# Kernel optimization log

Hardware: AMD Instinct MI355X
Metric: run time of the kernel (lower is better)

Reference implementation:

```python
import jax, jax.numpy as jnp
import numpy as np

DT = 0.1
DEATH_THRESHOLD = 0.05


def setup_inputs() -> dict:
    key = jax.random.key(0)
    ks = jax.random.split(key, 12)
    B, S, DE, DM, DC, DEPTH = 1, 4096, 256, 64, 64, 4
    DIN = DE + DC
    w_scale = 0.02  # keeps pre-softmax scores in a sane range
    return {
        "e": jax.random.normal(ks[0], (B, S, DE), jnp.float32),
        "E": jax.random.uniform(ks[1], (B, S, 1), jnp.float32),
        "P": jax.random.uniform(ks[2], (B, S, 1), jnp.float32),
        "G": jax.random.normal(ks[3], (B, S, 1), jnp.float32),
        "m": jax.random.uniform(ks[4], (B, S, DM), jnp.float32),
        "c": jax.random.normal(ks[5], (B, S, DC), jnp.float32),
        "l": jax.random.uniform(ks[6], (B, S, 1), jnp.float32),
        "wq": jax.random.normal(ks[7], (DEPTH, DIN, DE), jnp.float32) * w_scale,
        "bq": jnp.zeros((DEPTH, DE), jnp.float32),
        "wk": jax.random.normal(ks[8], (DEPTH, DIN, DE), jnp.float32) * w_scale,
        "bk": jnp.zeros((DEPTH, DE), jnp.float32),
        "wv": jax.random.normal(ks[9], (DEPTH, DIN, DE), jnp.float32) * w_scale,
        "bv": jnp.zeros((DEPTH, DE), jnp.float32),
        "alpha": jnp.full((DEPTH,), 1.0, jnp.float32),
        "beta": jnp.full((DEPTH,), 0.5, jnp.float32),
        "gamma": jnp.full((DEPTH,), 0.2, jnp.float32),
        "basal": jnp.full((DEPTH,), 0.05, jnp.float32),
    }


def reference(e, E, P, G, m, c, l, wq, bq, wk, bk, wv, bv, alpha, beta, gamma, basal):
    depth = wq.shape[0]
    scale = 1.0 / np.sqrt(wq.shape[-1]).astype(np.float32)
    for i in range(depth):
        # --- OuterTrans: multiplicatively-masked self-attention ---
        x = jnp.concatenate([e, c], axis=-1)                 # [B,S,DE+DC]
        q = x @ wq[i] + bq[i]
        k = x @ wk[i] + bk[i]
        v = x @ wv[i] + bv[i]
        scores = jnp.einsum("bsd,btd->bst", q, k) * scale    # [B,S,S]
        membrane = jnp.einsum("bsd,btd->bst", m, m)          # [B,S,S]
        lifespan = jnp.einsum("bsd,btd->bst", l, l)          # [B,S,S]
        attn = jax.nn.softmax(scores * membrane * lifespan, axis=-1)
        h_tilde = jnp.einsum("bst,btd->bsd", attn, v)        # [B,S,DE]
        e = e + h_tilde
        # --- ThermodynamicODE (elementwise per-token update) ---
        S_in = jnp.sum(h_tilde * h_tilde, axis=-1, keepdims=True)  # ||h||^2 [B,S,1]
        PE = P * E
        P_new = jax.nn.relu(P + (alpha[i] * S_in - beta[i] * PE) * DT)
        E_new = jax.nn.relu(E + (basal[i] - gamma[i] * PE) * DT)
        m_target = jax.nn.sigmoid(E_new - P_new)             # [B,S,1] broadcast to m
        G = G + (0.1 * E_new - 0.5 * P_new) * DT
        l_decay = 0.01 + 0.5 * jax.nn.relu(P_new - 2.0)
        m = 0.9 * m + 0.1 * m_target
        l = jnp.clip(l - l_decay * DT, 0.0, 1.0)
        E, P = E_new, P_new
    # Dynamic pruning: jit-compatible variant -> zero-mask dead cells instead of
    # data-dependent slicing; also return alive_mask and num_died.
    alive = l > DEATH_THRESHOLD                              # [B,S,1] bool
    af = alive.astype(e.dtype)
    num_died = e.shape[1] - jnp.sum(alive.astype(jnp.int32))
    return (e * af, E * af, P * af, G * af, m * af, c * af, l * af,
            alive[0, :, 0], num_died)
```

## Files before the change

kernel.cpp:

```cpp
#include <hip/hip_runtime.h>
#include <hip/hip_bf16.h>
#include <math.h>

#define SS 4096
#define DE 256
#define DM 64
#define DC 64
#define DIN 320
#define DEPTH 4
#define DT_C 0.1f
#define NSPLIT 12
#define BK 32
#define EXP_SHIFT 8.0f

typedef float f32x4_t __attribute__((ext_vector_type(4)));
typedef __bf16 bf16x8_t __attribute__((ext_vector_type(8)));

#define MFMA_BF16(A, B, C) __builtin_amdgcn_mfma_f32_16x16x32_bf16((A), (B), (C), 0, 0, 0)

#define OFF_E     (SS*DE)
#define OFF_P     (OFF_E + SS)
#define OFF_G     (OFF_P + SS)
#define OFF_M     (OFF_G + SS)
#define OFF_C     (OFF_M + SS*DM)
#define OFF_L     (OFF_C + SS*DM)
#define OFF_ALIVE (OFF_L + SS)
#define OFF_DIED  (OFF_ALIVE + SS)

#define WS_EWS   0
#define WS_MWS   (WS_EWS  + SS*DE)
#define WS_EE    (WS_MWS  + SS*DM)
#define WS_PP    (WS_EE   + SS)
#define WS_GG    (WS_PP   + SS)
#define WS_LL    (WS_GG   + SS)
#define WS_PL    (WS_LL   + SS)
#define WS_POB   (WS_PL   + NSPLIT*SS)
#define WS_XB    (WS_POB  + NSPLIT*SS*DE/2)
#define WS_QB    (WS_XB   + SS*DIN/2)
#define WS_KB    (WS_QB   + SS*DE/2)
#define WS_VTB   (WS_KB   + SS*DE/2)
#define WS_MB    (WS_VTB  + SS*DE/2)
#define WS_WT    (WS_MB   + SS*DM/2)
#define WS_SEM   (WS_WT   + 3*DEPTH*DE*DIN/2)

#define KT_STR 264
#define VT_STR 40

__global__ __launch_bounds__(256) void transpose_w_kernel(
    const float* __restrict__ wq, const float* __restrict__ wk, const float* __restrict__ wv,
    __hip_bfloat16* __restrict__ wt)
{
    const int zd = blockIdx.z;
    const int z = zd >> 2;
    const float* src = (z == 0 ? wq : (z == 1 ? wk : wv)) + (size_t)(zd & 3) * DIN * DE;
    __shared__ float t[32][33];
    const int k0 = blockIdx.x * 32;
    const int n0 = blockIdx.y * 32;
    const int tr = threadIdx.x >> 5;
    const int tc = threadIdx.x & 31;
    #pragma unroll
    for (int p = 0; p < 4; ++p)
        t[p*8 + tr][tc] = src[(size_t)(k0 + p*8 + tr) * DE + n0 + tc];
    __syncthreads();
    #pragma unroll
    for (int p = 0; p < 4; ++p) {
        int n = n0 + p*8 + tr;
        int k = k0 + tc;
        wt[((size_t)zd * DE + n) * DIN + k] = __float2bfloat16(t[tc][p*8 + tr]);
    }
}

__global__ __launch_bounds__(256) void init_kernel(
    const float* __restrict__ e_in, const float* __restrict__ c_in,
    const float* __restrict__ E_in, const float* __restrict__ P_in,
    const float* __restrict__ G_in, const float* __restrict__ l_in,
    const float* __restrict__ m_in,
    float* __restrict__ e_ws, __hip_bfloat16* __restrict__ xb,
    float* __restrict__ E_ws, float* __restrict__ P_ws, float* __restrict__ G_ws,
    float* __restrict__ l_ws, float* __restrict__ m_ws, __hip_bfloat16* __restrict__ mb,
    int* __restrict__ counters)
{
    const int row = blockIdx.x;
    const int tid = threadIdx.x;
    const float v = e_in[(size_t)row * DE + tid];
    e_ws[(size_t)row * DE + tid] = v;
    xb[(size_t)row * DIN + tid] = __float2bfloat16(v);
    if (tid < DC) {
        xb[(size_t)row * DIN + DE + tid] = __float2bfloat16(c_in[(size_t)row * DC + tid]);
        const float mv = m_in[(size_t)row * DM + tid];
        m_ws[(size_t)row * DM + tid] = mv;
        mb[(size_t)row * DM + tid] = __float2bfloat16(mv);
    }
    if (tid == 0) {
        E_ws[row] = E_in[row];
        P_ws[row] = P_in[row];
        G_ws[row] = G_in[row];
        l_ws[row] = l_in[row];
    }
    if (row == 0 && tid < 2) counters[tid] = 0;
}

__global__ __launch_bounds__(256, 2) void projc_kernel(
    const __hip_bfloat16* __restrict__ part_ob, const float* __restrict__ part_l,
    float* __restrict__ e_ws, __hip_bfloat16* __restrict__ xb,
    float* __restrict__ E_ws, float* __restrict__ P_ws, float* __restrict__ G_ws,
    float* __restrict__ m_ws, __hip_bfloat16* __restrict__ mb, float* __restrict__ l_ws,
    const float* __restrict__ alpha, const float* __restrict__ beta,
    const float* __restrict__ gamma_, const float* __restrict__ basal,
    const __hip_bfloat16* __restrict__ wt,
    const float* __restrict__ bq, const float* __restrict__ bk, const float* __restrict__ bv,
    __hip_bfloat16* __restrict__ qb, __hip_bfloat16* __restrict__ kb, __hip_bfloat16* __restrict__ vtb,
    int layer)
{
    const int id = blockIdx.x;
    const int xcd = id & 7, inner = id >> 3;
    const int qblk = (xcd << 3) | (inner >> 2);
    const int rb = qblk * 4 + (inner & 3);
    const int tid = threadIdx.x;

    if (layer > 0) {
        const int wc = tid >> 6, lane = tid & 63;
        const int lp = layer - 1;
        const float a = alpha[lp], bb = beta[lp], gm = gamma_[lp], bas = basal[lp];
        #pragma unroll
        for (int rr = 0; rr < 4; ++rr) {
            const int row = rb * 16 + wc * 4 + rr;
            const int qb2 = row >> 6, wa = (row >> 4) & 3, quada = (row >> 2) & 3, ra = row & 3;
            float L = 0.f;
            #pragma unroll
            for (int s = 0; s < NSPLIT; ++s) L += part_l[s * SS + row];
            const float invL = 1.0f / L;
            const int ct = lane >> 2;
            const int base_off = (ct * 64 + quada * 16 + (lane & 3) * 4) * 4;
            float o[4] = {0.f, 0.f, 0.f, 0.f};
            #pragma unroll
            for (int s = 0; s < NSPLIT; ++s) {
                const size_t region = ((size_t)((s * (SS / 64) + qb2) * 4 + wa)) * 4096;
                const ushort* pp = (const ushort*)(part_ob + region) + base_off;
                ushort vals[16];
                *(uint4*)&vals[0] = *(const uint4*)pp;
                *(uint4*)&vals[8] = *(const uint4*)(pp + 8);
                #pragma unroll
                for (int j = 0; j < 4; ++j)
                    o[j] += __uint_as_float(((unsigned)vals[j * 4 + ra]) << 16);
            }
            const float h0 = o[0] * invL, h1 = o[1] * invL, h2 = o[2] * invL, h3 = o[3] * invL;
            float4 ev = *(float4*)&e_ws[(size_t)row * DE + lane * 4];
            ev.x += h0; ev.y += h1; ev.z += h2; ev.w += h3;
            *(float4*)&e_ws[(size_t)row * DE + lane * 4] = ev;
            __hip_bfloat16 x4[4] = {__float2bfloat16(ev.x), __float2bfloat16(ev.y),
                                    __float2bfloat16(ev.z), __float2bfloat16(ev.w)};
            *(uint2*)&xb[(size_t)row * DIN + lane * 4] = *(uint2*)x4;

            float ssq = h0*h0 + h1*h1 + h2*h2 + h3*h3;
            #pragma unroll
            for (int mask = 1; mask < 64; mask <<= 1) ssq += __shfl_xor(ssq, mask);

            const float E = E_ws[row], P = P_ws[row];
            const float PE = P * E;
            const float Pn = fmaxf(0.f, P + (a * ssq - bb * PE) * DT_C);
            const float En = fmaxf(0.f, E + (bas - gm * PE) * DT_C);
            const float mtg = 1.f / (1.f + __expf(-(En - Pn)));
            const size_t mi = (size_t)row * DM + lane;
            const float mv = 0.9f * m_ws[mi] + 0.1f * mtg;
            m_ws[mi] = mv;
            mb[mi] = __float2bfloat16(mv);
            if (lane == 0) {
                E_ws[row] = En;
                P_ws[row] = Pn;
                G_ws[row] = G_ws[row] + (0.1f * En - 0.5f * Pn) * DT_C;
                const float ldec = 0.01f + 0.5f * fmaxf(0.f, Pn - 2.0f);
                const float lv = l_ws[row] - ldec * DT_C;
                l_ws[row] = fminf(1.f, fmaxf(0.f, lv));
            }
        }
        __syncthreads();
    }

    const int w = tid >> 6, lane = tid & 63;
    const int m = lane & 15, quad = lane >> 4;
    const int row0 = rb * 16;

    bf16x8_t xa[10];
    #pragma unroll
    for (int kk = 0; kk < 10; ++kk)
        xa[kk] = *(const bf16x8_t*)&xb[(size_t)(row0 + m) * DIN + kk * 32 + quad * 8];

    f32x4_t acc[12];
    #pragma unroll
    for (int nt = 0; nt < 12; ++nt) acc[nt] = (f32x4_t){0.f, 0.f, 0.f, 0.f};

    #pragma unroll
    for (int kk = 0; kk < 10; ++kk) {
        #pragma unroll
        for (int nt = 0; nt < 12; ++nt) {
            const int gcol = w * 192 + nt * 16 + m;
            const int z = gcol >> 8, col = gcol & 255;
            bf16x8_t bfrag = *(const bf16x8_t*)&wt[((size_t)(z * DEPTH + layer) * DE + col) * DIN + kk * 32 + quad * 8];
            acc[nt] = MFMA_BF16(xa[kk], bfrag, acc[nt]);
        }
    }
    #pragma unroll
    for (int nt = 0; nt < 12; ++nt) {
        const int gcol = w * 192 + nt * 16 + m;
        const int z = gcol >> 8, col = gcol & 255;
        const float* bias = (z == 0 ? bq : (z == 1 ? bk : bv)) + (size_t)layer * DE;
        const float b = bias[col];
        #pragma unroll
        for (int r = 0; r < 4; ++r) {
            const int row = row0 + quad * 4 + r;
            const __hip_bfloat16 h = __float2bfloat16(acc[nt][r] + b);
            if (z == 0)      qb[(size_t)row * DE + col] = h;
            else if (z == 1) kb[(size_t)row * DE + col] = h;
            else             vtb[(size_t)col * SS + row] = h;
        }
    }
}

__global__ __launch_bounds__(256, 3) void attn_mfma_kernel(
    const __hip_bfloat16* __restrict__ qb, const __hip_bfloat16* __restrict__ kb,
    const __hip_bfloat16* __restrict__ vtb, const __hip_bfloat16* __restrict__ mb,
    const float* __restrict__ l_ws,
    __hip_bfloat16* __restrict__ part_ob, float* __restrict__ part_l)
{
    __shared__ __align__(16) __hip_bfloat16 kt[32 * KT_STR];
    __shared__ __align__(16) __hip_bfloat16 vt[256 * VT_STR];

    const int id = blockIdx.x;
    const int split = id >> 6;
    const int rid = id & 63;
    const int qblk = (rid & 7) * 8 + (rid >> 3);

    const int tid = threadIdx.x;
    const int w = tid >> 6, lane = tid & 63;
    const int n = lane & 15, quad = lane >> 4;
    const int row0 = qblk * 64 + w * 16;

    bf16x8_t qa[8];
    #pragma unroll
    for (int kk = 0; kk < 8; ++kk)
        qa[kk] = *(const bf16x8_t*)&qb[(size_t)(row0 + n) * DE + kk * 32 + quad * 8];
    bf16x8_t ma[2];
    #pragma unroll
    for (int kk = 0; kk < 2; ++kk)
        ma[kk] = *(const bf16x8_t*)&mb[(size_t)(row0 + n) * DM + kk * 32 + quad * 8];
    const float lqs = l_ws[row0 + n] * 0.0625f;

    f32x4_t oacc[16];
    #pragma unroll
    for (int ct = 0; ct < 16; ++ct) oacc[ct] = (f32x4_t){0.f, 0.f, 0.f, 0.f};
    float plsum = 0.f;
    const f32x4_t zf4 = (f32x4_t){0.f, 0.f, 0.f, 0.f};

    const int k_row = tid >> 5, k_g = tid & 31;
    const int v_col = tid >> 2, v_seg = tid & 3;
    const int v_base = (v_seg & 1) * 16 + (v_seg >> 1) * 4;

    const int it_begin = (split * 128) / NSPLIT;
    const int it_end   = ((split + 1) * 128) / NSPLIT;

    for (int it = it_begin; it < it_end; ++it) {
        const int t0 = it * BK;
        __syncthreads();
        #pragma unroll
        for (int p = 0; p < 4; ++p) {
            const int row = k_row + p * 8;
            *(float4*)&kt[row * KT_STR + k_g * 8] = *(const float4*)&kb[(size_t)(t0 + row) * DE + k_g * 8];
        }
        #pragma unroll
        for (int p = 0; p < 4; ++p) {
            const int col = v_col + p * 64;
            const float4 f = *(const float4*)&vtb[(size_t)col * SS + t0 + v_seg * 8];
            *(float2*)&vt[col * VT_STR + v_base]     = make_float2(f.x, f.y);
            *(float2*)&vt[col * VT_STR + v_base + 8] = make_float2(f.z, f.w);
        }
        __syncthreads();

        const bf16x8_t mf00 = *(const bf16x8_t*)&mb[(size_t)(t0 + n) * DM + quad * 8];
        const bf16x8_t mf01 = *(const bf16x8_t*)&mb[(size_t)(t0 + n) * DM + 32 + quad * 8];
        const bf16x8_t mf10 = *(const bf16x8_t*)&mb[(size_t)(t0 + n + 16) * DM + quad * 8];
        const bf16x8_t mf11 = *(const bf16x8_t*)&mb[(size_t)(t0 + n + 16) * DM + 32 + quad * 8];
        const float4 lk0 = *(const float4*)&l_ws[t0 + quad * 4];
        const float4 lk1 = *(const float4*)&l_ws[t0 + 16 + quad * 4];

        f32x4_t s0a = zf4, s0b = zf4, s1a = zf4, s1b = zf4;
        #pragma unroll
        for (int kk = 0; kk < 4; ++kk) {
            bf16x8_t k0 = *(const bf16x8_t*)&kt[n * KT_STR + kk * 32 + quad * 8];
            bf16x8_t k1 = *(const bf16x8_t*)&kt[(n + 16) * KT_STR + kk * 32 + quad * 8];
            s0a = MFMA_BF16(k0, qa[kk], s0a);
            s1a = MFMA_BF16(k1, qa[kk], s1a);
        }
        #pragma unroll
        for (int kk = 4; kk < 8; ++kk) {
            bf16x8_t k0 = *(const bf16x8_t*)&kt[n * KT_STR + kk * 32 + quad * 8];
            bf16x8_t k1 = *(const bf16x8_t*)&kt[(n + 16) * KT_STR + kk * 32 + quad * 8];
            s0b = MFMA_BF16(k0, qa[kk], s0b);
            s1b = MFMA_BF16(k1, qa[kk], s1b);
        }
        const f32x4_t st0 = s0a + s0b;
        const f32x4_t st1 = s1a + s1b;

        f32x4_t mm0 = MFMA_BF16(mf00, ma[0], zf4);
        mm0 = MFMA_BF16(mf01, ma[1], mm0);
        f32x4_t mm1 = MFMA_BF16(mf10, ma[0], zf4);
        mm1 = MFMA_BF16(mf11, ma[1], mm1);

        bf16x8_t pa;
        #pragma unroll
        for (int r = 0; r < 4; ++r) {
            const float x0 = st0[r] * lqs * lk0[r] * mm0[r];
            const float x1 = st1[r] * lqs * lk1[r] * mm1[r];
            const float p0 = __expf(x0 - EXP_SHIFT);
            const float p1 = __expf(x1 - EXP_SHIFT);
            plsum += p0 + p1;
            pa[r]     = (__bf16)p0;
            pa[4 + r] = (__bf16)p1;
        }

        #pragma unroll
        for (int ct = 0; ct < 16; ++ct) {
            bf16x8_t vb = *(const bf16x8_t*)&vt[(ct * 16 + n) * VT_STR + quad * 8];
            oacc[ct] = MFMA_BF16(pa, vb, oacc[ct]);
        }
    }

    plsum += __shfl_xor(plsum, 16);
    plsum += __shfl_xor(plsum, 32);
    if (lane < 16)
        part_l[split * SS + row0 + lane] = plsum;

    __hip_bfloat16* dst = part_ob + ((size_t)((split * (SS / 64) + qblk) * 4 + w)) * 4096;
    #pragma unroll
    for (int ct = 0; ct < 16; ++ct) {
        __hip_bfloat16 h4[4];
        #pragma unroll
        for (int r = 0; r < 4; ++r) h4[r] = __float2bfloat16(oacc[ct][r]);
        *(uint2*)&dst[(ct * 64 + lane) * 4] = *(uint2*)h4;
    }
}

__global__ __launch_bounds__(256) void finalizec_kernel(
    const __hip_bfloat16* __restrict__ part_ob, const float* __restrict__ part_l,
    const float* __restrict__ e_ws,
    const float* __restrict__ E_ws, const float* __restrict__ P_ws, const float* __restrict__ G_ws,
    const float* __restrict__ m_ws, const float* __restrict__ c_in, const float* __restrict__ l_ws,
    const float* __restrict__ alpha, const float* __restrict__ beta,
    const float* __restrict__ gamma_, const float* __restrict__ basal,
    float* __restrict__ out, int* __restrict__ counters)
{
    const int id = blockIdx.x;
    const int xcd = id & 7, inner = id >> 3;
    const int qblk = (xcd << 3) | (inner >> 2);
    const int rb = qblk * 4 + (inner & 3);
    const int tid = threadIdx.x;
    const int wc = tid >> 6, lane = tid & 63;

    const int lp = DEPTH - 1;
    const float a = alpha[lp], bb = beta[lp], gm = gamma_[lp], bas = basal[lp];

    __shared__ int s_alive[4];
    int alive_cnt = 0;

    #pragma unroll
    for (int rr = 0; rr < 4; ++rr) {
        const int row = rb * 16 + wc * 4 + rr;
        const int qb2 = row >> 6, wa = (row >> 4) & 3, quada = (row >> 2) & 3, ra = row & 3;
        float L = 0.f;
        #pragma unroll
        for (int s = 0; s < NSPLIT; ++s) L += part_l[s * SS + row];
        const float invL = 1.0f / L;
        const int ct = lane >> 2;
        const int base_off = (ct * 64 + quada * 16 + (lane & 3) * 4) * 4;
        float o[4] = {0.f, 0.f, 0.f, 0.f};
        #pragma unroll
        for (int s = 0; s < NSPLIT; ++s) {
            const size_t region = ((size_t)((s * (SS / 64) + qb2) * 4 + wa)) * 4096;
            const ushort* pp = (const ushort*)(part_ob + region) + base_off;
            ushort vals[16];
            *(uint4*)&vals[0] = *(const uint4*)pp;
            *(uint4*)&vals[8] = *(const uint4*)(pp + 8);
            #pragma unroll
            for (int j = 0; j < 4; ++j)
                o[j] += __uint_as_float(((unsigned)vals[j * 4 + ra]) << 16);
        }
        const float h0 = o[0] * invL, h1 = o[1] * invL, h2 = o[2] * invL, h3 = o[3] * invL;
        float4 ev = *(const float4*)&e_ws[(size_t)row * DE + lane * 4];
        ev.x += h0; ev.y += h1; ev.z += h2; ev.w += h3;

        float ssq = h0*h0 + h1*h1 + h2*h2 + h3*h3;
        #pragma unroll
        for (int mask = 1; mask < 64; mask <<= 1) ssq += __shfl_xor(ssq, mask);

        const float E = E_ws[row], P = P_ws[row];
        const float PE = P * E;
        const float Pn = fmaxf(0.f, P + (a * ssq - bb * PE) * DT_C);
        const float En = fmaxf(0.f, E + (bas - gm * PE) * DT_C);
        const float mtg = 1.f / (1.f + __expf(-(En - Pn)));
        const float mv = 0.9f * m_ws[(size_t)row * DM + lane] + 0.1f * mtg;
        const float Gn = G_ws[row] + (0.1f * En - 0.5f * Pn) * DT_C;
        const float ldec = 0.01f + 0.5f * fmaxf(0.f, Pn - 2.0f);
        const float lv = fminf(1.f, fmaxf(0.f, l_ws[row] - ldec * DT_C));
        const float af = (lv > 0.05f) ? 1.f : 0.f;

        float4 eo = make_float4(ev.x * af, ev.y * af, ev.z * af, ev.w * af);
        *(float4*)&out[(size_t)row * DE + lane * 4] = eo;
        out[OFF_M + (size_t)row * DM + lane] = mv * af;
        out[OFF_C + (size_t)row * DM + lane] = c_in[(size_t)row * DM + lane] * af;
        if (lane == 0) {
            out[OFF_E + row] = En * af;
            out[OFF_P + row] = Pn * af;
            out[OFF_G + row] = Gn * af;
            out[OFF_L + row] = lv * af;
            out[OFF_ALIVE + row] = af;
            alive_cnt += (af > 0.f) ? 1 : 0;
        }
    }

    if (lane == 0) s_alive[wc] = alive_cnt;
    __syncthreads();
    if (tid == 0) {
        const int blk_alive = s_alive[0] + s_alive[1] + s_alive[2] + s_alive[3];
        atomicAdd(&counters[0], blk_alive);
        __threadfence();
        const int old = atomicAdd(&counters[1], 1);
        if (old == 255) {
            __threadfence();
            const int tot = atomicAdd(&counters[0], 0);
            out[OFF_DIED] = (float)(SS - tot);
        }
    }
}

extern "C" void kernel_launch(void* const* d_in, const int* in_sizes, int n_in,
                              void* d_out, int out_size, void* d_ws, size_t ws_size,
                              hipStream_t stream) {
    const float* e_in = (const float*)d_in[0];
    const float* E_in = (const float*)d_in[1];
    const float* P_in = (const float*)d_in[2];
    const float* G_in = (const float*)d_in[3];
    const float* m_in = (const float*)d_in[4];
    const float* c_in = (const float*)d_in[5];
    const float* l_in = (const float*)d_in[6];
    const float* wq = (const float*)d_in[7];
    const float* bq = (const float*)d_in[8];
    const float* wk = (const float*)d_in[9];
    const float* bk = (const float*)d_in[10];
    const float* wv = (const float*)d_in[11];
    const float* bv = (const float*)d_in[12];
    const float* alpha = (const float*)d_in[13];
    const float* beta  = (const float*)d_in[14];
    const float* gamma_ = (const float*)d_in[15];
    const float* basal = (const float*)d_in[16];
    float* out = (float*)d_out;
    float* ws = (float*)d_ws;

    float* e_ws = ws + WS_EWS;
    float* m_ws = ws + WS_MWS;
    float* E_ws = ws + WS_EE;
    float* P_ws = ws + WS_PP;
    float* G_ws = ws + WS_GG;
    float* l_ws = ws + WS_LL;
    float* part_l = ws + WS_PL;
    __hip_bfloat16* part_ob = (__hip_bfloat16*)(ws + WS_POB);
    __hip_bfloat16* xb  = (__hip_bfloat16*)(ws + WS_XB);
    __hip_bfloat16* qb  = (__hip_bfloat16*)(ws + WS_QB);
    __hip_bfloat16* kb  = (__hip_bfloat16*)(ws + WS_KB);
    __hip_bfloat16* vtb = (__hip_bfloat16*)(ws + WS_VTB);
    __hip_bfloat16* mb  = (__hip_bfloat16*)(ws + WS_MB);
    __hip_bfloat16* wt  = (__hip_bfloat16*)(ws + WS_WT);
    int* counters = (int*)(ws + WS_SEM);

    transpose_w_kernel<<<dim3(DIN/32, DE/32, 12), 256, 0, stream>>>(wq, wk, wv, wt);
    init_kernel<<<dim3(SS), 256, 0, stream>>>(
        e_in, c_in, E_in, P_in, G_in, l_in, m_in,
        e_ws, xb, E_ws, P_ws, G_ws, l_ws, m_ws, mb, counters);

    for (int layer = 0; layer < DEPTH; ++layer) {
        projc_kernel<<<dim3(SS/16), 256, 0, stream>>>(
            part_ob, part_l, e_ws, xb, E_ws, P_ws, G_ws, m_ws, mb, l_ws,
            alpha, beta, gamma_, basal, wt, bq, bk, bv, qb, kb, vtb, layer);
        attn_mfma_kernel<<<dim3((SS/64) * NSPLIT), 256, 0, stream>>>(
            qb, kb, vtb, mb, l_ws, part_ob, part_l);
    }
    finalizec_kernel<<<dim3(SS/16), 256, 0, stream>>>(
        part_ob, part_l, e_ws, E_ws, P_ws, G_ws, m_ws, c_in, l_ws,
        alpha, beta, gamma_, basal, out, counters);
}
```

Measured before the change: 469.6 us.

## Split fused combine+projection into LDS-tiled GEMM and separate combine kernel

```diff
diff --git a/kernel.cpp b/kernel.cpp
--- a/kernel.cpp
+++ b/kernel.cpp
@@ -45,6 +45,7 @@
 
 #define KT_STR 264
 #define VT_STR 40
+#define PJ_STR 72
 
 __global__ __launch_bounds__(256) void transpose_w_kernel(
     const float* __restrict__ wq, const float* __restrict__ wk, const float* __restrict__ wv,
@@ -100,120 +101,81 @@
     if (row == 0 && tid < 2) counters[tid] = 0;
 }
 
-__global__ __launch_bounds__(256, 2) void projc_kernel(
-    const __hip_bfloat16* __restrict__ part_ob, const float* __restrict__ part_l,
-    float* __restrict__ e_ws, __hip_bfloat16* __restrict__ xb,
-    float* __restrict__ E_ws, float* __restrict__ P_ws, float* __restrict__ G_ws,
-    float* __restrict__ m_ws, __hip_bfloat16* __restrict__ mb, float* __restrict__ l_ws,
-    const float* __restrict__ alpha, const float* __restrict__ beta,
-    const float* __restrict__ gamma_, const float* __restrict__ basal,
-    const __hip_bfloat16* __restrict__ wt,
+__global__ __launch_bounds__(256, 4) void proj_gemm_kernel(
+    const __hip_bfloat16* __restrict__ xb, const __hip_bfloat16* __restrict__ wt,
     const float* __restrict__ bq, const float* __restrict__ bk, const float* __restrict__ bv,
     __hip_bfloat16* __restrict__ qb, __hip_bfloat16* __restrict__ kb, __hip_bfloat16* __restrict__ vtb,
     int layer)
 {
-    const int id = blockIdx.x;
-    const int xcd = id & 7, inner = id >> 3;
-    const int qblk = (xcd << 3) | (inner >> 2);
-    const int rb = qblk * 4 + (inner & 3);
+    __shared__ __align__(16) __hip_bfloat16 at[64 * PJ_STR];
+    __shared__ __align__(16) __hip_bfloat16 bt[64 * PJ_STR];
+    __shared__ __align__(16) __hip_bfloat16 tt[64 * PJ_STR];
+
+    const int mt = blockIdx.x;
+    const int nt4 = blockIdx.y;
+    const int row0 = mt * 64;
+    const int z = nt4 >> 2;
+    const int coln0 = (nt4 & 3) * 64;
+    const __hip_bfloat16* wrow = wt + ((size_t)(z * DEPTH + layer) * DE + coln0) * DIN;
+
     const int tid = threadIdx.x;
-
-    if (layer > 0) {
-        const int wc = tid >> 6, lane = tid & 63;
-        const int lp = layer - 1;
-        const float a = alpha[lp], bb = beta[lp], gm = gamma_[lp], bas = basal[lp];
-        #pragma unroll
-        for (int rr = 0; rr < 4; ++rr) {
-            const int row = rb * 16 + wc * 4 + rr;
-            const int qb2 = row >> 6, wa = (row >> 4) & 3, quada = (row >> 2) & 3, ra = row & 3;
-            float L = 0.f;
+    const int w = tid >> 6, lane = tid & 63;
+    const int ml = lane & 15, quad = lane >> 4;
+    const int s_r = tid >> 2, s_g = tid & 3;
+
+    f32x4_t acc[4];
+    #pragma unroll
+    for (int nt = 0; nt < 4; ++nt) acc[nt] = (f32x4_t){0.f, 0.f, 0.f, 0.f};
+
+    for (int k0 = 0; k0 < DIN; k0 += 64) {
+        __syncthreads();
+        {
+            const __hip_bfloat16* src = &xb[(size_t)(row0 + s_r) * DIN + k0 + s_g * 16];
+            *(float4*)&at[s_r * PJ_STR + s_g * 16]     = *(const float4*)src;
+            *(float4*)&at[s_r * PJ_STR + s_g * 16 + 8] = *(const float4*)(src + 8);
+        }
+        {
+            const __hip_bfloat16* src = &wrow[(size_t)s_r * DIN + k0 + s_g * 16];
+            *(float4*)&bt[s_r * PJ_STR + s_g * 16]     = *(const float4*)src;
+            *(float4*)&bt[s_r * PJ_STR + s_g * 16 + 8] = *(const float4*)(src + 8);
+        }
+        __syncthreads();
+        #pragma unroll
+        for (int kk = 0; kk < 2; ++kk) {
+            const bf16x8_t a = *(const bf16x8_t*)&at[(w * 16 + ml) * PJ_STR + kk * 32 + quad * 8];
             #pragma unroll
-            for (int s = 0; s < NSPLIT; ++s) L += part_l[s * SS + row];
-            const float invL = 1.0f / L;
-            const int ct = lane >> 2;
-            const int base_off = (ct * 64 + quada * 16 + (lane & 3) * 4) * 4;
-            float o[4] = {0.f, 0.f, 0.f, 0.f};
+            for (int nt = 0; nt < 4; ++nt) {
+                const bf16x8_t b = *(const bf16x8_t*)&bt[(nt * 16 + ml) * PJ_STR + kk * 32 + quad * 8];
+                acc[nt] = MFMA_BF16(a, b, acc[nt]);
+            }
+        }
+    }
+
+    const float* bias = (z == 0 ? bq : (z == 1 ? bk : bv)) + (size_t)layer * DE;
+    if (z < 2) {
+        __hip_bfloat16* O = (z == 0 ? qb : kb);
+        #pragma unroll
+        for (int nt = 0; nt < 4; ++nt) {
+            const int col = coln0 + nt * 16 + ml;
+            const float b = bias[col];
             #pragma unroll
-            for (int s = 0; s < NSPLIT; ++s) {
-                const size_t region = ((size_t)((s * (SS / 64) + qb2) * 4 + wa)) * 4096;
-                const ushort* pp = (const ushort*)(part_ob + region) + base_off;
-                ushort vals[16];
-                *(uint4*)&vals[0] = *(const uint4*)pp;
-                *(uint4*)&vals[8] = *(const uint4*)(pp + 8);
-                #pragma unroll
-                for (int j = 0; j < 4; ++j)
-                    o[j] += __uint_as_float(((unsigned)vals[j * 4 + ra]) << 16);
-            }
-            const float h0 = o[0] * invL, h1 = o[1] * invL, h2 = o[2] * invL, h3 = o[3] * invL;
-            float4 ev = *(float4*)&e_ws[(size_t)row * DE + lane * 4];
-            ev.x += h0; ev.y += h1; ev.z += h2; ev.w += h3;
-            *(float4*)&e_ws[(size_t)row * DE + lane * 4] = ev;
-            __hip_bfloat16 x4[4] = {__float2bfloat16(ev.x), __float2bfloat16(ev.y),
-                                    __float2bfloat16(ev.z), __float2bfloat16(ev.w)};
-            *(uint2*)&xb[(size_t)row * DIN + lane * 4] = *(uint2*)x4;
-
-            float ssq = h0*h0 + h1*h1 + h2*h2 + h3*h3;
+            for (int r = 0; r < 4; ++r)
+                O[(size_t)(row0 + w * 16 + quad * 4 + r) * DE + col] = __float2bfloat16(acc[nt][r] + b);
+        }
+    } else {
+        #pragma unroll
+        for (int nt = 0; nt < 4; ++nt) {
+            const int n = nt * 16 + ml;
+            const float b = bias[coln0 + n];
             #pragma unroll
-            for (int mask = 1; mask < 64; mask <<= 1) ssq += __shfl_xor(ssq, mask);
-
-            const float E = E_ws[row], P = P_ws[row];
-            const float PE = P * E;
-            const float Pn = fmaxf(0.f, P + (a * ssq - bb * PE) * DT_C);
-            const float En = fmaxf(0.f, E + (bas - gm * PE) * DT_C);
-            const float mtg = 1.f / (1.f + __expf(-(En - Pn)));
-            const size_t mi = (size_t)row * DM + lane;
-            const float mv = 0.9f * m_ws[mi] + 0.1f * mtg;
-            m_ws[mi] = mv;
-            mb[mi] = __float2bfloat16(mv);
-            if (lane == 0) {
-                E_ws[row] = En;
-                P_ws[row] = Pn;
-                G_ws[row] = G_ws[row] + (0.1f * En - 0.5f * Pn) * DT_C;
-                const float ldec = 0.01f + 0.5f * fmaxf(0.f, Pn - 2.0f);
-                const float lv = l_ws[row] - ldec * DT_C;
-                l_ws[row] = fminf(1.f, fmaxf(0.f, lv));
-            }
+            for (int r = 0; r < 4; ++r)
+                tt[n * PJ_STR + w * 16 + quad * 4 + r] = __float2bfloat16(acc[nt][r] + b);
         }
         __syncthreads();
-    }
-
-    const int w = tid >> 6, lane = tid & 63;
-    const int m = lane & 15, quad = lane >> 4;
-    const int row0 = rb * 16;
-
-    bf16x8_t xa[10];
-    #pragma unroll
-    for (int kk = 0; kk < 10; ++kk)
-        xa[kk] = *(const bf16x8_t*)&xb[(size_t)(row0 + m) * DIN + kk * 32 + quad * 8];
-
-    f32x4_t acc[12];
-    #pragma unroll
-    for (int nt = 0; nt < 12; ++nt) acc[nt] = (f32x4_t){0.f, 0.f, 0.f, 0.f};
-
-    #pragma unroll
-    for (int kk = 0; kk < 10; ++kk) {
-        #pragma unroll
-        for (int nt = 0; nt < 12; ++nt) {
-            const int gcol = w * 192 + nt * 16 + m;
-            const int z = gcol >> 8, col = gcol & 255;
-            bf16x8_t bfrag = *(const bf16x8_t*)&wt[((size_t)(z * DEPTH + layer) * DE + col) * DIN + kk * 32 + quad * 8];
-            acc[nt] = MFMA_BF16(xa[kk], bfrag, acc[nt]);
-        }
-    }
-    #pragma unroll
-    for (int nt = 0; nt < 12; ++nt) {
-        const int gcol = w * 192 + nt * 16 + m;
-        const int z = gcol >> 8, col = gcol & 255;
-        const float* bias = (z == 0 ? bq : (z == 1 ? bk : bv)) + (size_t)layer * DE;
-        const float b = bias[col];
-        #pragma unroll
-        for (int r = 0; r < 4; ++r) {
-            const int row = row0 + quad * 4 + r;
-            const __hip_bfloat16 h = __float2bfloat16(acc[nt][r] + b);
-            if (z == 0)      qb[(size_t)row * DE + col] = h;
-            else if (z == 1) kb[(size_t)row * DE + col] = h;
-            else             vtb[(size_t)col * SS + row] = h;
-        }
+        const int c = tid >> 2, seg = tid & 3;
+        __hip_bfloat16* dst = &vtb[(size_t)(coln0 + c) * SS + row0 + seg * 16];
+        *(float4*)dst       = *(const float4*)&tt[c * PJ_STR + seg * 16];
+        *(float4*)(dst + 8) = *(const float4*)&tt[c * PJ_STR + seg * 16 + 8];
     }
 }
 
@@ -337,6 +299,72 @@
         #pragma unroll
         for (int r = 0; r < 4; ++r) h4[r] = __float2bfloat16(oacc[ct][r]);
         *(uint2*)&dst[(ct * 64 + lane) * 4] = *(uint2*)h4;
+    }
+}
+
+__global__ __launch_bounds__(256) void combine_kernel(
+    const __hip_bfloat16* __restrict__ part_ob, const float* __restrict__ part_l,
+    float* __restrict__ e_ws, __hip_bfloat16* __restrict__ xb,
+    float* __restrict__ E_ws, float* __restrict__ P_ws, float* __restrict__ G_ws,
+    float* __restrict__ m_ws, __hip_bfloat16* __restrict__ mb, float* __restrict__ l_ws,
+    const float* __restrict__ alpha, const float* __restrict__ beta,
+    const float* __restrict__ gamma_, const float* __restrict__ basal, int layer)
+{
+    const int wc = threadIdx.x >> 6, lane = threadIdx.x & 63;
+    const int row = blockIdx.x * 4 + wc;
+    const int qblk = row >> 6, wa = (row >> 4) & 3, quada = (row >> 2) & 3, ra = row & 3;
+
+    float L = 0.f;
+    #pragma unroll
+    for (int s = 0; s < NSPLIT; ++s) L += part_l[s * SS + row];
+    const float invL = 1.0f / L;
+
+    const int ct = lane >> 2;
+    const int base_off = (ct * 64 + quada * 16 + (lane & 3) * 4) * 4;
+    float o[4] = {0.f, 0.f, 0.f, 0.f};
+    #pragma unroll
+    for (int s = 0; s < NSPLIT; ++s) {
+        const size_t region = ((size_t)((s * (SS / 64) + qblk) * 4 + wa)) * 4096;
+        const ushort* pp = (const ushort*)(part_ob + region) + base_off;
+        ushort vals[16];
+        *(uint4*)&vals[0] = *(const uint4*)pp;
+        *(uint4*)&vals[8] = *(const uint4*)(pp + 8);
+        #pragma unroll
+        for (int j = 0; j < 4; ++j)
+            o[j] += __uint_as_float(((unsigned)vals[j * 4 + ra]) << 16);
+    }
+    float h0 = o[0] * invL, h1 = o[1] * invL, h2 = o[2] * invL, h3 = o[3] * invL;
+
+    float4 ev = *(float4*)&e_ws[(size_t)row * DE + lane * 4];
+    ev.x += h0; ev.y += h1; ev.z += h2; ev.w += h3;
+    *(float4*)&e_ws[(size_t)row * DE + lane * 4] = ev;
+    {
+        __hip_bfloat16 x4[4] = {__float2bfloat16(ev.x), __float2bfloat16(ev.y),
+                                __float2bfloat16(ev.z), __float2bfloat16(ev.w)};
+        *(uint2*)&xb[(size_t)row * DIN + lane * 4] = *(uint2*)x4;
+    }
+
+    float ssq = h0*h0 + h1*h1 + h2*h2 + h3*h3;
+    #pragma unroll
+    for (int mask = 1; mask < 64; mask <<= 1) ssq += __shfl_xor(ssq, mask);
+
+    const float a = alpha[layer], b = beta[layer], gm = gamma_[layer], bas = basal[layer];
+    const float E = E_ws[row], P = P_ws[row];
+    const float PE = P * E;
+    const float Pn = fmaxf(0.f, P + (a * ssq - b * PE) * DT_C);
+    const float En = fmaxf(0.f, E + (bas - gm * PE) * DT_C);
+    const float mtg = 1.f / (1.f + __expf(-(En - Pn)));
+    const size_t mi = (size_t)row * DM + lane;
+    const float mv = 0.9f * m_ws[mi] + 0.1f * mtg;
+    m_ws[mi] = mv;
+    mb[mi] = __float2bfloat16(mv);
+    if (lane == 0) {
+        E_ws[row] = En;
+        P_ws[row] = Pn;
+        G_ws[row] = G_ws[row] + (0.1f * En - 0.5f * Pn) * DT_C;
+        const float ldec = 0.01f + 0.5f * fmaxf(0.f, Pn - 2.0f);
+        const float lv = l_ws[row] - ldec * DT_C;
+        l_ws[row] = fminf(1.f, fmaxf(0.f, lv));
     }
 }
 
@@ -349,10 +377,7 @@
     const float* __restrict__ gamma_, const float* __restrict__ basal,
     float* __restrict__ out, int* __restrict__ counters)
 {
-    const int id = blockIdx.x;
-    const int xcd = id & 7, inner = id >> 3;
-    const int qblk = (xcd << 3) | (inner >> 2);
-    const int rb = qblk * 4 + (inner & 3);
+    const int rb = blockIdx.x;
     const int tid = threadIdx.x;
     const int wc = tid >> 6, lane = tid & 63;
 
@@ -477,11 +502,14 @@
         e_ws, xb, E_ws, P_ws, G_ws, l_ws, m_ws, mb, counters);
 
     for (int layer = 0; layer < DEPTH; ++layer) {
-        projc_kernel<<<dim3(SS/16), 256, 0, stream>>>(
-            part_ob, part_l, e_ws, xb, E_ws, P_ws, G_ws, m_ws, mb, l_ws,
-            alpha, beta, gamma_, basal, wt, bq, bk, bv, qb, kb, vtb, layer);
+        proj_gemm_kernel<<<dim3(SS/64, 12), 256, 0, stream>>>(
+            xb, wt, bq, bk, bv, qb, kb, vtb, layer);
         attn_mfma_kernel<<<dim3((SS/64) * NSPLIT), 256, 0, stream>>>(
             qb, kb, vtb, mb, l_ws, part_ob, part_l);
+        if (layer < DEPTH - 1)
+            combine_kernel<<<dim3(SS/4), 256, 0, stream>>>(
+                part_ob, part_l, e_ws, xb, E_ws, P_ws, G_ws, m_ws, mb, l_ws,
+                alpha, beta, gamma_, basal, layer);
     }
     finalizec_kernel<<<dim3(SS/16), 256, 0, stream>>>(
         part_ob, part_l, e_ws, E_ws, P_ws, G_ws, m_ws, c_in, l_ws,
```

Result: faster. 415.3 us (-11.6%).
